# Kernel tuning notes

Hardware: AMD Instinct MI355X
Metric: run time of the kernel (lower is better)

The kernel has to match this reference:

```python
import jax, jax.numpy as jnp
import numpy as np

B, L, H, W, C = 2, 32, 16, 16, 32  # L must equal channels for the view() to be consistent
CH = L  # conv channel count


def setup_inputs() -> dict:
    key = jax.random.key(0)
    k1, k2, k3, k4, k5 = jax.random.split(key, 5)
    return {
        "inputs": jax.random.normal(k1, (B, L, H, W, C), dtype=jnp.float32),
        "W1": jax.random.normal(k2, (CH // 2, CH), dtype=jnp.float32) * 0.1,
        "b1": jax.random.normal(k3, (CH // 2,), dtype=jnp.float32) * 0.1,
        "W2": jax.random.normal(k4, (CH, CH), dtype=jnp.float32) * 0.1,
        "b2": jax.random.normal(k5, (CH,), dtype=jnp.float32) * 0.1,
        "gamma": jnp.ones((1,), dtype=jnp.float32),
    }


def reference(inputs, W1, b1, W2, b2, gamma):
    b, l, h, w, c = inputs.shape
    n = l * h * w  # flattened 'spatial' positions after the (buggy-but-faithful) reshape
    # conv1x1 over dim-1 (torch Conv3d treats dim-1 as channels)
    x1 = jnp.einsum('ol,blhwc->bohwc', W1, inputs) + b1[None, :, None, None, None]
    # permute (0,4,1,2,3) then view(b, c//2, l*h*w)
    x1 = jnp.transpose(x1, (0, 4, 1, 2, 3)).reshape(b, c // 2, n)
    # attn[b, i, j] = sum_k x1[b, k, i] * x1[b, k, j]; softmax over last dim
    attn = jax.nn.softmax(jnp.einsum('bki,bkj->bij', x1, x1), axis=-1)  # [b, n, n]
    x2 = jnp.einsum('ol,blhwc->bohwc', W2, inputs) + b2[None, :, None, None, None]
    x2 = jnp.transpose(x2, (0, 4, 1, 2, 3)).reshape(b, c, n)
    # x2 @ attn^T : out[b, c, i] = sum_j x2[b, c, j] * attn[b, i, j]
    out = jnp.einsum('bcj,bij->bci', x2, attn)
    out = jnp.transpose(out.reshape(b, c, l, h, w), (0, 2, 3, 4, 1))
    return out * gamma + inputs
```

## Files before the change

### kernel.cpp

```cpp
#include <hip/hip_runtime.h>
#include <hip/hip_bf16.h>
#include <math.h>

typedef __bf16 bf16x8 __attribute__((ext_vector_type(8)));
typedef __bf16 bf16x2 __attribute__((ext_vector_type(2)));
typedef float  floatx16 __attribute__((ext_vector_type(16)));
typedef unsigned u32x4 __attribute__((ext_vector_type(4)));

#define KQ_ELEMS (2 * 8192 * 16)
#define OPART_OFF 1572864
#define SQRT_LOG2E 1.2011224087864498f
#define LSPLIT 4

__global__ __launch_bounds__(512) void proj_kernel(
    const float* __restrict__ in, const float* __restrict__ W1,
    const float* __restrict__ b1, const float* __restrict__ W2,
    const float* __restrict__ b2,
    __hip_bfloat16* __restrict__ Kq, __hip_bfloat16* __restrict__ Vswz)
{
    __shared__ float Xs[32][32];
    __shared__ float W1s[16 * 32];
    __shared__ float W2s[32 * 32];
    const int t = threadIdx.x;
    const int bid = blockIdx.x;
    const int b = bid >> 8;
    const int hw = bid & 255;

    {
        int l = t >> 4, cs = (t & 15) * 2;
        float2 v = *(const float2*)(in + (((size_t)b * 32 + l) * 256 + hw) * 32 + cs);
        *(float2*)&Xs[l][cs] = v;
    }
    if (t < 128) *(float4*)&W1s[t * 4] = *(const float4*)(W1 + t * 4);
    if (t < 256) *(float4*)&W2s[t * 4] = *(const float4*)(W2 + t * 4);
    __syncthreads();

    const int c = t & 31;
    const int g = t >> 5;

    {
        int o = g;
        float a0 = b1[o], a1 = 0.f;
#pragma unroll
        for (int l = 0; l < 16; ++l) {
            a0 += W1s[o * 32 + l] * Xs[l][c];
            a1 += W1s[o * 32 + 16 + l] * Xs[16 + l][c];
        }
        float acc = a0 + a1;
        int k = c >> 1;
        int i = (c & 1) * 4096 + o * 256 + hw;
        Kq[((size_t)b * 8192 + i) * 16 + k] = __float2bfloat16(acc * SQRT_LOG2E);
    }
#pragma unroll
    for (int oo = 0; oo < 2; ++oo) {
        int o = g * 2 + oo;
        float a0 = b2[o], a1 = 0.f;
#pragma unroll
        for (int l = 0; l < 16; ++l) {
            a0 += W2s[o * 32 + l] * Xs[l][c];
            a1 += W2s[o * 32 + 16 + l] * Xs[16 + l][c];
        }
        float acc = a0 + a1;
        int jt = o * 8 + (hw >> 5);
        int f  = (hw >> 4) & 1;
        int hh = (hw >> 2) & 1;
        int idx = (hw & 3) | (((hw >> 3) & 1) << 2);
        Vswz[(size_t)b * 262144 + jt * 1024 + f * 512 + hh * 256 + c * 8 + idx] =
            __float2bfloat16(acc);
    }
}

__global__ __launch_bounds__(256, 5) void flash_kernel(
    const __hip_bfloat16* __restrict__ Kq, const __hip_bfloat16* __restrict__ Vswz,
    __hip_bfloat16* __restrict__ Opart, float* __restrict__ Lpart)
{
    const int t = threadIdx.x;
    const int lane = t & 63;
    const int wv = t >> 6;
    const int m = lane & 31;
    const int h = lane >> 5;

    const int bid = blockIdx.x;
    const int s = bid & ((1 << LSPLIT) - 1);
    const int itile = (bid >> LSPLIT) & 63;
    const int b = bid >> (LSPLIT + 6);
    const int i0 = itile * 128 + wv * 32;
    const int niter = (8192 >> LSPLIT) >> 5;
    const int jt0 = s * niter;

    const __hip_bfloat16* Kb = Kq + (size_t)b * 8192 * 16;
    const __hip_bfloat16* Vb = Vswz + (size_t)b * 262144 + h * 256 + m * 8;

    const bf16x8 bq = *(const bf16x8*)(Kb + (size_t)(i0 + m) * 16 + h * 8);

    floatx16 oa = {};
    float l0 = 0.f, l1 = 0.f, l2 = 0.f, l3 = 0.f;

    bf16x8 ak = *(const bf16x8*)(Kb + (size_t)(jt0 * 32 + m) * 16 + h * 8);
    bf16x8 vb0 = *(const bf16x8*)(Vb + (size_t)jt0 * 1024 + 0);
    bf16x8 vb1 = *(const bf16x8*)(Vb + (size_t)jt0 * 1024 + 512);

#pragma unroll 2
    for (int it = 0; it < niter; ++it) {
        const bf16x8 cak = ak;
        const bf16x8 cv0 = vb0, cv1 = vb1;
        if (it + 1 < niter) {
            const int jn = jt0 + it + 1;
            ak  = *(const bf16x8*)(Kb + (size_t)(jn * 32 + m) * 16 + h * 8);
            vb0 = *(const bf16x8*)(Vb + (size_t)jn * 1024 + 0);
            vb1 = *(const bf16x8*)(Vb + (size_t)jn * 1024 + 512);
        }

        floatx16 sc = __builtin_amdgcn_mfma_f32_32x32x16_bf16(cak, bq, (floatx16){}, 0, 0, 0);

#pragma unroll
        for (int half = 0; half < 2; ++half) {
            u32x4 pau;
#pragma unroll
            for (int gg = 0; gg < 2; ++gg) {
                const int g = half * 2 + gg;
                float e0 = __builtin_amdgcn_exp2f(sc[4 * g + 0]);
                float e1 = __builtin_amdgcn_exp2f(sc[4 * g + 1]);
                float e2 = __builtin_amdgcn_exp2f(sc[4 * g + 2]);
                float e3 = __builtin_amdgcn_exp2f(sc[4 * g + 3]);
                l0 += e0; l1 += e1; l2 += e2; l3 += e3;
#if defined(__has_builtin) && __has_builtin(__builtin_amdgcn_cvt_pk_bf16_f32)
                bf16x2 pk0 = __builtin_amdgcn_cvt_pk_bf16_f32(e0, e1);
                bf16x2 pk1 = __builtin_amdgcn_cvt_pk_bf16_f32(e2, e3);
#else
                bf16x2 pk0 = {(__bf16)e0, (__bf16)e1};
                bf16x2 pk1 = {(__bf16)e2, (__bf16)e3};
#endif
                pau[gg * 2 + 0] = __builtin_bit_cast(unsigned, pk0);
                pau[gg * 2 + 1] = __builtin_bit_cast(unsigned, pk1);
            }
            bf16x8 pa = __builtin_bit_cast(bf16x8, pau);
            oa = __builtin_amdgcn_mfma_f32_32x32x16_bf16(pa, half ? cv1 : cv0, oa, 0, 0, 0);
        }
    }

    float l = (l0 + l1) + (l2 + l3);
    l += __shfl_xor(l, 32);
    const float rinv = __builtin_amdgcn_rcpf(l);

#pragma unroll
    for (int r = 0; r < 16; ++r) {
        int iloc = (r & 3) + 8 * (r >> 2) + 4 * h;
        float lr = __shfl(rinv, iloc);
        size_t row = (size_t)b * 8192 + i0 + iloc;
        Opart[((row << LSPLIT) | s) * 32 + m] = __float2bfloat16(oa[r] * lr);
    }
    if (h == 0)
        Lpart[(((size_t)b * 8192 + i0 + m) << LSPLIT) | s] = l;
}

__global__ __launch_bounds__(256) void combine_kernel(
    const unsigned short* __restrict__ Opart, const float* __restrict__ Lpart,
    const float* __restrict__ in, const float* __restrict__ gamma,
    float* __restrict__ out)
{
    const int gid = blockIdx.x * 256 + threadIdx.x;
    const int row = gid >> 4;
    const int c2 = (gid & 15) * 2;
    const unsigned short* op = Opart + (((size_t)row << LSPLIT)) * 32 + c2;
    const float* lp = Lpart + ((size_t)row << LSPLIT);
    float ls[1 << LSPLIT];
#pragma unroll
    for (int q = 0; q < (1 << LSPLIT) / 4; ++q) {
        float4 lv = *(const float4*)(lp + q * 4);
        ls[q * 4 + 0] = lv.x; ls[q * 4 + 1] = lv.y;
        ls[q * 4 + 2] = lv.z; ls[q * 4 + 3] = lv.w;
    }
    float ax = 0.f, ay = 0.f;
    float lsum = 0.f;
#pragma unroll
    for (int s = 0; s < (1 << LSPLIT); ++s) {
        ushort2 u = *(const ushort2*)(op + s * 32);
        float l = ls[s];
        ax += l * __uint_as_float((unsigned)u.x << 16);
        ay += l * __uint_as_float((unsigned)u.y << 16);
        lsum += l;
    }
    const size_t base = (size_t)row * 32 + c2;
    float2 x = *(const float2*)(in + base);
    const float gl = gamma[0] / lsum;
    float2 r;
    r.x = ax * gl + x.x;
    r.y = ay * gl + x.y;
    *(float2*)(out + base) = r;
}

extern "C" void kernel_launch(void* const* d_in, const int* in_sizes, int n_in,
                              void* d_out, int out_size, void* d_ws, size_t ws_size,
                              hipStream_t stream) {
    const float* in = (const float*)d_in[0];
    const float* W1 = (const float*)d_in[1];
    const float* b1 = (const float*)d_in[2];
    const float* W2 = (const float*)d_in[3];
    const float* b2 = (const float*)d_in[4];
    const float* gamma = (const float*)d_in[5];
    float* out = (float*)d_out;

    __hip_bfloat16* Kq = (__hip_bfloat16*)d_ws;
    __hip_bfloat16* Vswz = Kq + KQ_ELEMS;
    __hip_bfloat16* Opart = (__hip_bfloat16*)((char*)d_ws + OPART_OFF);
    float* Lpart = (float*)(Opart + ((size_t)16384 << LSPLIT) * 32);

    proj_kernel<<<512, 512, 0, stream>>>(in, W1, b1, W2, b2, Kq, Vswz);
    flash_kernel<<<2 * 64 * (1 << LSPLIT), 256, 0, stream>>>(Kq, Vswz, Opart, Lpart);
    combine_kernel<<<1024, 256, 0, stream>>>((const unsigned short*)Opart, Lpart, in, gamma, out);
}
```

Before: 98.13 us.

## Process two key tiles per iteration and halve the key split in flash kernel

The flash loop now handles two 32-key tiles per iteration, issuing both score MFMAs up front and prefetching the next pair's K and V fragments, so more independent MFMA and exp work is available to hide latency. The key-dimension split drops from 16 to 8 partitions, which halves the partial outputs written and combined but leaves fewer, longer blocks. Launch bounds go from 5 to 4 waves-per-EU to allow the extra registers the doubled prefetch needs, at the cost of occupancy.

```diff
diff --git a/kernel.cpp b/kernel.cpp
--- a/kernel.cpp
+++ b/kernel.cpp
@@ -10,7 +10,7 @@
 #define KQ_ELEMS (2 * 8192 * 16)
 #define OPART_OFF 1572864
 #define SQRT_LOG2E 1.2011224087864498f
-#define LSPLIT 4
+#define LSPLIT 3
 
 __global__ __launch_bounds__(512) void proj_kernel(
     const float* __restrict__ in, const float* __restrict__ W1,
@@ -70,7 +70,7 @@
     }
 }
 
-__global__ __launch_bounds__(256, 5) void flash_kernel(
+__global__ __launch_bounds__(256, 4) void flash_kernel(
     const __hip_bfloat16* __restrict__ Kq, const __hip_bfloat16* __restrict__ Vswz,
     __hip_bfloat16* __restrict__ Opart, float* __restrict__ Lpart)
 {
@@ -86,6 +86,7 @@
     const int b = bid >> (LSPLIT + 6);
     const int i0 = itile * 128 + wv * 32;
     const int niter = (8192 >> LSPLIT) >> 5;
+    const int npair = niter >> 1;
     const int jt0 = s * niter;
 
     const __hip_bfloat16* Kb = Kq + (size_t)b * 8192 * 16;
@@ -96,22 +97,29 @@
     floatx16 oa = {};
     float l0 = 0.f, l1 = 0.f, l2 = 0.f, l3 = 0.f;
 
-    bf16x8 ak = *(const bf16x8*)(Kb + (size_t)(jt0 * 32 + m) * 16 + h * 8);
-    bf16x8 vb0 = *(const bf16x8*)(Vb + (size_t)jt0 * 1024 + 0);
-    bf16x8 vb1 = *(const bf16x8*)(Vb + (size_t)jt0 * 1024 + 512);
-
-#pragma unroll 2
-    for (int it = 0; it < niter; ++it) {
-        const bf16x8 cak = ak;
-        const bf16x8 cv0 = vb0, cv1 = vb1;
-        if (it + 1 < niter) {
-            const int jn = jt0 + it + 1;
-            ak  = *(const bf16x8*)(Kb + (size_t)(jn * 32 + m) * 16 + h * 8);
-            vb0 = *(const bf16x8*)(Vb + (size_t)jn * 1024 + 0);
-            vb1 = *(const bf16x8*)(Vb + (size_t)jn * 1024 + 512);
-        }
-
-        floatx16 sc = __builtin_amdgcn_mfma_f32_32x32x16_bf16(cak, bq, (floatx16){}, 0, 0, 0);
+    bf16x8 ak0 = *(const bf16x8*)(Kb + (size_t)(jt0 * 32 + m) * 16 + h * 8);
+    bf16x8 ak1 = *(const bf16x8*)(Kb + (size_t)((jt0 + 1) * 32 + m) * 16 + h * 8);
+    bf16x8 va0 = *(const bf16x8*)(Vb + (size_t)jt0 * 1024 + 0);
+    bf16x8 va1 = *(const bf16x8*)(Vb + (size_t)jt0 * 1024 + 512);
+    bf16x8 vc0 = *(const bf16x8*)(Vb + (size_t)(jt0 + 1) * 1024 + 0);
+    bf16x8 vc1 = *(const bf16x8*)(Vb + (size_t)(jt0 + 1) * 1024 + 512);
+
+#pragma unroll 1
+    for (int ip = 0; ip < npair; ++ip) {
+        const bf16x8 cak0 = ak0, cak1 = ak1;
+        const bf16x8 cva0 = va0, cva1 = va1, cvc0 = vc0, cvc1 = vc1;
+        if (ip + 1 < npair) {
+            const int jn = jt0 + 2 * (ip + 1);
+            ak0 = *(const bf16x8*)(Kb + (size_t)(jn * 32 + m) * 16 + h * 8);
+            ak1 = *(const bf16x8*)(Kb + (size_t)((jn + 1) * 32 + m) * 16 + h * 8);
+            va0 = *(const bf16x8*)(Vb + (size_t)jn * 1024 + 0);
+            va1 = *(const bf16x8*)(Vb + (size_t)jn * 1024 + 512);
+            vc0 = *(const bf16x8*)(Vb + (size_t)(jn + 1) * 1024 + 0);
+            vc1 = *(const bf16x8*)(Vb + (size_t)(jn + 1) * 1024 + 512);
+        }
+
+        floatx16 sc0 = __builtin_amdgcn_mfma_f32_32x32x16_bf16(cak0, bq, (floatx16){}, 0, 0, 0);
+        floatx16 sc1 = __builtin_amdgcn_mfma_f32_32x32x16_bf16(cak1, bq, (floatx16){}, 0, 0, 0);
 
 #pragma unroll
         for (int half = 0; half < 2; ++half) {
@@ -119,10 +127,10 @@
 #pragma unroll
             for (int gg = 0; gg < 2; ++gg) {
                 const int g = half * 2 + gg;
-                float e0 = __builtin_amdgcn_exp2f(sc[4 * g + 0]);
-                float e1 = __builtin_amdgcn_exp2f(sc[4 * g + 1]);
-                float e2 = __builtin_amdgcn_exp2f(sc[4 * g + 2]);
-                float e3 = __builtin_amdgcn_exp2f(sc[4 * g + 3]);
+                float e0 = __builtin_amdgcn_exp2f(sc0[4 * g + 0]);
+                float e1 = __builtin_amdgcn_exp2f(sc0[4 * g + 1]);
+                float e2 = __builtin_amdgcn_exp2f(sc0[4 * g + 2]);
+                float e3 = __builtin_amdgcn_exp2f(sc0[4 * g + 3]);
                 l0 += e0; l1 += e1; l2 += e2; l3 += e3;
 #if defined(__has_builtin) && __has_builtin(__builtin_amdgcn_cvt_pk_bf16_f32)
                 bf16x2 pk0 = __builtin_amdgcn_cvt_pk_bf16_f32(e0, e1);
@@ -135,7 +143,31 @@
                 pau[gg * 2 + 1] = __builtin_bit_cast(unsigned, pk1);
             }
             bf16x8 pa = __builtin_bit_cast(bf16x8, pau);
-            oa = __builtin_amdgcn_mfma_f32_32x32x16_bf16(pa, half ? cv1 : cv0, oa, 0, 0, 0);
+            oa = __builtin_amdgcn_mfma_f32_32x32x16_bf16(pa, half ? cva1 : cva0, oa, 0, 0, 0);
+        }
+#pragma unroll
+        for (int half = 0; half < 2; ++half) {
+            u32x4 pau;
+#pragma unroll
+            for (int gg = 0; gg < 2; ++gg) {
+                const int g = half * 2 + gg;
+                float e0 = __builtin_amdgcn_exp2f(sc1[4 * g + 0]);
+                float e1 = __builtin_amdgcn_exp2f(sc1[4 * g + 1]);
+                float e2 = __builtin_amdgcn_exp2f(sc1[4 * g + 2]);
+                float e3 = __builtin_amdgcn_exp2f(sc1[4 * g + 3]);
+                l0 += e0; l1 += e1; l2 += e2; l3 += e3;
+#if defined(__has_builtin) && __has_builtin(__builtin_amdgcn_cvt_pk_bf16_f32)
+                bf16x2 pk0 = __builtin_amdgcn_cvt_pk_bf16_f32(e0, e1);
+                bf16x2 pk1 = __builtin_amdgcn_cvt_pk_bf16_f32(e2, e3);
+#else
+                bf16x2 pk0 = {(__bf16)e0, (__bf16)e1};
+                bf16x2 pk1 = {(__bf16)e2, (__bf16)e3};
+#endif
+                pau[gg * 2 + 0] = __builtin_bit_cast(unsigned, pk0);
+                pau[gg * 2 + 1] = __builtin_bit_cast(unsigned, pk1);
+            }
+            bf16x8 pa = __builtin_bit_cast(bf16x8, pau);
+            oa = __builtin_amdgcn_mfma_f32_32x32x16_bf16(pa, half ? cvc1 : cvc0, oa, 0, 0, 0);
         }
     }
 
```

Result: no change. 96.29 us (-1.9%).
